# Performance work log

Measured on AMD Instinct MI355X. Metric: run time of the kernel, lower is better.

The kernel has to match this reference:

```python
import jax, jax.numpy as jnp
import numpy as np
import math

N_HEADS = 16
D_EMB = 1024
D_HEAD = D_EMB // N_HEADS


def setup_inputs() -> dict:
    key = jax.random.key(0)
    ks = jax.random.split(key, 5)
    scale_in = 1.0 / math.sqrt(D_EMB)
    x = jax.random.normal(ks[0], (2, 2048, D_EMB), dtype=jnp.float32)
    w_in = jax.random.uniform(ks[1], (3 * D_EMB, D_EMB), dtype=jnp.float32, minval=-scale_in, maxval=scale_in)
    b_in = jax.random.uniform(ks[2], (3 * D_EMB,), dtype=jnp.float32, minval=-scale_in, maxval=scale_in)
    w_out = jax.random.uniform(ks[3], (D_EMB, D_EMB), dtype=jnp.float32, minval=-scale_in, maxval=scale_in)
    b_out = jax.random.uniform(ks[4], (D_EMB,), dtype=jnp.float32, minval=-scale_in, maxval=scale_in)
    return {"x": x, "w_in": w_in, "b_in": b_in, "w_out": w_out, "b_out": b_out, "apply_mask": 1}


def reference(x, w_in, b_in, w_out, b_out, apply_mask):
    B, S, D = x.shape
    # fused QKV projection: torch Linear uses y = x @ W^T + b
    qkv = jnp.einsum('bsd,ed->bse', x, w_in) + b_in  # [B,S,3D]
    q, k, v = jnp.split(qkv, 3, axis=-1)
    # [B,H,S,Dh]
    q = q.reshape(B, S, N_HEADS, D_HEAD).transpose(0, 2, 1, 3)
    k = k.reshape(B, S, N_HEADS, D_HEAD).transpose(0, 2, 1, 3)
    v = v.reshape(B, S, N_HEADS, D_HEAD).transpose(0, 2, 1, 3)
    w = jnp.einsum('bhqd,bhkd->bhqk', q, k)  # [B,H,S,S]
    if apply_mask:
        causal = jnp.triu(jnp.ones((S, S), dtype=bool), k=1)
        w = jnp.where(causal, -jnp.inf, w)
    w = w / jnp.sqrt(jnp.float32(D_HEAD)).astype(w.dtype)
    w = jax.nn.softmax(w, axis=-1)
    score = jnp.einsum('bhqk,bhkd->bhqd', w, v)  # [B,H,S,Dh]
    score = score.transpose(0, 2, 1, 3).reshape(B, S, D)
    return jnp.einsum('bsd,ed->bse', score, w_out) + b_out
```

## Files before the change

kernel.cpp:

```cpp
#include <hip/hip_runtime.h>
#include <stdint.h>

#define DEMB 1024
#define NHEAD 16
#define DHEAD 64
#define SEQ 2048
#define MROWS 4096

typedef __bf16 bf16x8 __attribute__((ext_vector_type(8)));
typedef float f32x4 __attribute__((ext_vector_type(4)));
typedef unsigned short u16;

#define LOG2E 1.44269504088896340736f

__device__ __forceinline__ u16 f2b(float f) {
  uint32_t u = __builtin_bit_cast(uint32_t, f);
  u += 0x7fffu + ((u >> 16) & 1u);
  return (u16)(u >> 16);
}

__device__ __forceinline__ f32x4 mfma16(bf16x8 a, bf16x8 b, f32x4 c) {
  return __builtin_amdgcn_mfma_f32_16x16x32_bf16(a, b, c, 0, 0, 0);
}

__device__ __forceinline__ void gload_lds16(const void* g, void* l) {
  __builtin_amdgcn_global_load_lds(
      (__attribute__((address_space(1))) unsigned int*)(g),
      (__attribute__((address_space(3))) unsigned int*)(l), 16, 0, 0);
}

__device__ __forceinline__ void tile_barrier() {
  __builtin_amdgcn_sched_barrier(0);
  asm volatile("s_waitcnt vmcnt(0) lgkmcnt(0)" ::: "memory");
  __builtin_amdgcn_s_barrier();
  __builtin_amdgcn_sched_barrier(0);
}

__global__ void cvt3_f32_bf16(const float* __restrict__ a, int na,
                              const float* __restrict__ b, int nb,
                              const float* __restrict__ c, int nc,
                              u16* __restrict__ da, u16* __restrict__ db,
                              u16* __restrict__ dc) {
  const int total = (na + nb + nc) >> 2;
  const int stride = gridDim.x * blockDim.x;
  for (int t = blockIdx.x * blockDim.x + threadIdx.x; t < total; t += stride) {
    int i = t << 2;
    const float* s;
    u16* d;
    if (i < na) {
      s = a + i; d = da + i;
    } else if (i < na + nb) {
      s = b + (i - na); d = db + (i - na);
    } else {
      s = c + (i - na - nb); d = dc + (i - na - nb);
    }
    float4 f = *(const float4*)s;
    ushort4 o;
    o.x = f2b(f.x); o.y = f2b(f.y); o.z = f2b(f.z); o.w = f2b(f.w);
    *(ushort4*)d = o;
  }
}

template <int EPI>
__global__ __launch_bounds__(256, 2) void gemm_nt(
    const u16* __restrict__ A, const u16* __restrict__ Bw,
    const float* __restrict__ bias, int K, int N,
    u16* __restrict__ q_out, u16* __restrict__ k_out, u16* __restrict__ v_out,
    float* __restrict__ f_out) {
  __shared__ __align__(16) u16 As[128 * 64];
  __shared__ __align__(16) u16 Bs[128 * 64];
  const int tid = threadIdx.x;
  const int w = tid >> 6;
  const int lane = tid & 63;
  const int wm = w >> 1, wn = w & 1;
  const int m0 = blockIdx.y * 128, n0 = blockIdx.x * 128;
  const int l16 = lane & 15, lg = lane >> 4;
  const int st_row = lane >> 3, st_slot = lane & 7;

  f32x4 acc[4][4] = {};

  for (int k0 = 0; k0 < K; k0 += 64) {
#pragma unroll
    for (int i = 0; i < 4; ++i) {
      const int chunk = (w << 2) | i;
      const int row = (chunk << 3) | st_row;
      const int scol = (st_slot ^ (row & 7)) << 3;
      gload_lds16(A + (size_t)(m0 + row) * K + k0 + scol, (char*)As + (chunk << 10));
      gload_lds16(Bw + (size_t)(n0 + row) * K + k0 + scol, (char*)Bs + (chunk << 10));
    }
    __syncthreads();
#pragma unroll
    for (int ks = 0; ks < 2; ++ks) {
      bf16x8 af[4], bfr[4];
#pragma unroll
      for (int mi = 0; mi < 4; ++mi) {
        const int row = wm * 64 + mi * 16 + l16;
        const int cb = ((ks << 6) | (lg << 4)) ^ ((row & 7) << 4);
        af[mi] = *(const bf16x8*)((const char*)As + row * 128 + cb);
      }
#pragma unroll
      for (int ni = 0; ni < 4; ++ni) {
        const int row = wn * 64 + ni * 16 + l16;
        const int cb = ((ks << 6) | (lg << 4)) ^ ((row & 7) << 4);
        bfr[ni] = *(const bf16x8*)((const char*)Bs + row * 128 + cb);
      }
#pragma unroll
      for (int mi = 0; mi < 4; ++mi)
#pragma unroll
        for (int ni = 0; ni < 4; ++ni)
          acc[mi][ni] = mfma16(af[mi], bfr[ni], acc[mi][ni]);
    }
    __syncthreads();
  }

#pragma unroll
  for (int ni = 0; ni < 4; ++ni) {
    const int n = n0 + wn * 64 + ni * 16 + l16;
    const float bv = bias[n];
    if (EPI == 0) {
      const int part = n >> 10;
      const int hh = (n >> 6) & 15;
      const int dh = n & 63;
      const float scl = (part == 0) ? (0.125f * LOG2E) : 1.0f;
      u16* dst = (part == 0) ? q_out : (part == 1) ? k_out : v_out;
#pragma unroll
      for (int mi = 0; mi < 4; ++mi) {
#pragma unroll
        for (int i = 0; i < 4; ++i) {
          const int m = m0 + wm * 64 + mi * 16 + (lg << 2) + i;
          const int bq = m >> 11, s = m & 2047;
          dst[((size_t)((bq << 4) | hh) * SEQ + s) * DHEAD + dh] = f2b((acc[mi][ni][i] + bv) * scl);
        }
      }
    } else {
#pragma unroll
      for (int mi = 0; mi < 4; ++mi)
#pragma unroll
        for (int i = 0; i < 4; ++i) {
          const int m = m0 + wm * 64 + mi * 16 + (lg << 2) + i;
          f_out[(size_t)m * N + n] = acc[mi][ni][i] + bv;
        }
    }
  }
}

__device__ __forceinline__ void stage_k(const u16* __restrict__ Kb, size_t base,
                                        int jt, u16* Ks, int w, int lane) {
  const int st_row = lane >> 3, st_slot = lane & 7;
#pragma unroll
  for (int i = 0; i < 2; ++i) {
    const int chunk = (w << 1) | i;
    const int row = (chunk << 3) | st_row;
    const int scol = (st_slot ^ (row & 7)) << 3;
    gload_lds16(Kb + base + (size_t)(jt * 64 + row) * DHEAD + scol, (char*)Ks + (chunk << 10));
  }
}

__device__ __forceinline__ int vswz(int rt) {
  return ((rt & 7) ^ ((rt >> 3) & 7)) << 4;
}

__device__ __forceinline__ void write_vt(u16* Vt, uint4 va, uint4 vb, int tid) {
  const int c0 = (tid & 7) << 3;
  const int vr0 = tid >> 3;
  const int vr1 = 32 + (tid >> 3);
  const u16* pa = (const u16*)&va;
  const u16* pb = (const u16*)&vb;
#pragma unroll
  for (int e = 0; e < 8; ++e) {
    const int rt = c0 + e;
    const int sw = vswz(rt);
    *(u16*)((char*)Vt + rt * 128 + ((vr0 << 1) ^ sw)) = pa[e];
    *(u16*)((char*)Vt + rt * 128 + ((vr1 << 1) ^ sw)) = pb[e];
  }
}

__global__ __launch_bounds__(256, 4) void attn_fwd(
    const u16* __restrict__ Qb, const u16* __restrict__ Kb,
    const u16* __restrict__ Vb, u16* __restrict__ Ob,
    const int* __restrict__ amask) {
  __shared__ __align__(16) u16 Ks[2][64 * 64];
  __shared__ __align__(16) u16 Vt[2][64 * 64];
  __shared__ __align__(16) uint32_t Ps[4][16 * 32];
  const int tid = threadIdx.x;
  const int w = tid >> 6, lane = tid & 63;
  const int l16 = lane & 15, lg = lane >> 4;

  const int id = blockIdx.x;
  const int xcd = id & 7;
  const int r = id >> 3;
  const int bh = (xcd << 2) | (r & 3);
  const int p = r >> 2;
  const int qiA = 31 - p, qiB = p;

  const size_t base = (size_t)bh * (SEQ * DHEAD);
  const bool causal = (amask[0] != 0);
  const int ntA = causal ? (qiA + 1) : (SEQ / 64);
  const int ntB = causal ? (qiB + 1) : (SEQ / 64);
  const int nt = ntA + ntB;
  const int b = bh >> 4, h = bh & 15;

  int qseg0 = qiA * 64;

  bf16x8 qf[2];
  {
    const u16* qp = Qb + base + (size_t)(qseg0 + (w << 4) + l16) * DHEAD + (lg << 3);
    qf[0] = *(const bf16x8*)qp;
    qf[1] = *(const bf16x8*)(qp + 32);
  }

  float mrow = -1e30f, lrow = 0.f;
  f32x4 oacc[4] = {};

  const int vcol = (tid & 7) << 3;
  const int vrow = tid >> 3;
  const int key = (l16 & 7) << 2;
  char* prow = (char*)(&Ps[w][0]) + l16 * 128;

  stage_k(Kb, base, 0, Ks[0], w, lane);
  {
    uint4 va = *(const uint4*)(Vb + base + (size_t)vrow * DHEAD + vcol);
    uint4 vb2 = *(const uint4*)(Vb + base + (size_t)(32 + vrow) * DHEAD + vcol);
    write_vt(Vt[0], va, vb2, tid);
  }
  tile_barrier();

  int cur = 0;
  for (int t = 0; t < nt; ++t) {
    const int j = (t >= ntA) ? (t - ntA) : t;
    const u16* Kcur = Ks[cur];
    const u16* Vcur = Vt[cur];
    const bool pre = (t + 1 < nt);
    uint4 vna = {}, vnb = {};
    if (pre) {
      const int jn = (t + 1 >= ntA) ? (t + 1 - ntA) : (t + 1);
      stage_k(Kb, base, jn, Ks[cur ^ 1], w, lane);
      const u16* vsrc = Vb + base + (size_t)jn * 64 * DHEAD;
      vna = *(const uint4*)(vsrc + (size_t)vrow * DHEAD + vcol);
      vnb = *(const uint4*)(vsrc + (size_t)(32 + vrow) * DHEAD + vcol);
    }

    f32x4 sv[4];
    __builtin_amdgcn_s_setprio(1);
#pragma unroll
    for (int nf = 0; nf < 4; ++nf) {
      const int row = nf * 16 + l16;
      const int sw = (row & 7) << 4;
      bf16x8 kf0 = *(const bf16x8*)((const char*)Kcur + row * 128 + ((lg << 4) ^ sw));
      bf16x8 kf1 = *(const bf16x8*)((const char*)Kcur + row * 128 + ((64 | (lg << 4)) ^ sw));
      f32x4 s = {};
      s = mfma16(kf0, qf[0], s);
      s = mfma16(kf1, qf[1], s);
      sv[nf] = s;
    }
    __builtin_amdgcn_s_setprio(0);

    const bool segEnd = (t == ntA - 1) || (t == nt - 1);
    if (causal && segEnd) {
      const int q = qseg0 + (w << 4) + l16;
#pragma unroll
      for (int nf = 0; nf < 4; ++nf)
#pragma unroll
        for (int i = 0; i < 4; ++i) {
          const int kv = j * 64 + nf * 16 + (lg << 2) + i;
          if (kv > q) sv[nf][i] = -1e30f;
        }
    }

    float tmax;
    {
      float t0 = fmaxf(fmaxf(sv[0][0], sv[0][1]), fmaxf(sv[0][2], sv[0][3]));
      float t1 = fmaxf(fmaxf(sv[1][0], sv[1][1]), fmaxf(sv[1][2], sv[1][3]));
      float t2 = fmaxf(fmaxf(sv[2][0], sv[2][1]), fmaxf(sv[2][2], sv[2][3]));
      float t3 = fmaxf(fmaxf(sv[3][0], sv[3][1]), fmaxf(sv[3][2], sv[3][3]));
      tmax = fmaxf(fmaxf(t0, t1), fmaxf(t2, t3));
      tmax = fmaxf(tmax, __shfl_xor(tmax, 16));
      tmax = fmaxf(tmax, __shfl_xor(tmax, 32));
    }

    if (__any(tmax > mrow + 8.0f)) {
      const float mnew = fmaxf(mrow, tmax);
      const float corr = exp2f(mrow - mnew);
      mrow = mnew;
      lrow *= corr;
#pragma unroll
      for (int df = 0; df < 4; ++df)
#pragma unroll
        for (int i = 0; i < 4; ++i) oacc[df][i] *= corr;
    }

    float psum = 0.f;
#pragma unroll
    for (int nf = 0; nf < 4; ++nf) {
      const float p0 = exp2f(sv[nf][0] - mrow);
      const float p1 = exp2f(sv[nf][1] - mrow);
      const float p2 = exp2f(sv[nf][2] - mrow);
      const float p3 = exp2f(sv[nf][3] - mrow);
      psum += (p0 + p1) + (p2 + p3);
      uint2 pk;
      pk.x = f2b(p0) | ((uint32_t)f2b(p1) << 16);
      pk.y = f2b(p2) | ((uint32_t)f2b(p3) << 16);
      const int word = ((nf << 3) | (lg << 1)) ^ key;
      *(uint2*)(prow + word * 4) = pk;
    }
    psum += __shfl_xor(psum, 16);
    psum += __shfl_xor(psum, 32);
    lrow += psum;

    bf16x8 pa0 = *(const bf16x8*)(prow + ((((lg << 2)) ^ key) << 2));
    bf16x8 pa1 = *(const bf16x8*)(prow + (((16 | (lg << 2)) ^ key) << 2));

    __builtin_amdgcn_s_setprio(1);
#pragma unroll
    for (int df = 0; df < 4; ++df) {
      const int row = df * 16 + l16;
      const int sw = vswz(row);
      bf16x8 vf0 = *(const bf16x8*)((const char*)Vcur + row * 128 + ((lg << 4) ^ sw));
      bf16x8 vf1 = *(const bf16x8*)((const char*)Vcur + row * 128 + ((64 | (lg << 4)) ^ sw));
      oacc[df] = mfma16(vf0, pa0, oacc[df]);
      oacc[df] = mfma16(vf1, pa1, oacc[df]);
    }
    __builtin_amdgcn_s_setprio(0);

    if (segEnd) {
      const float inv = 1.0f / lrow;
      const int s = qseg0 + (w << 4) + l16;
      u16* orow = Ob + (size_t)(b * SEQ + s) * DEMB + h * DHEAD;
#pragma unroll
      for (int df = 0; df < 4; ++df) {
        ushort4 o;
        o.x = f2b(oacc[df][0] * inv);
        o.y = f2b(oacc[df][1] * inv);
        o.z = f2b(oacc[df][2] * inv);
        o.w = f2b(oacc[df][3] * inv);
        *(ushort4*)(orow + df * 16 + (lg << 2)) = o;
      }
      if (t != nt - 1) {
        qseg0 = qiB * 64;
        mrow = -1e30f;
        lrow = 0.f;
#pragma unroll
        for (int df = 0; df < 4; ++df)
#pragma unroll
          for (int i = 0; i < 4; ++i) oacc[df][i] = 0.f;
        const u16* qp = Qb + base + (size_t)(qseg0 + (w << 4) + l16) * DHEAD + (lg << 3);
        qf[0] = *(const bf16x8*)qp;
        qf[1] = *(const bf16x8*)(qp + 32);
      }
    }

    if (pre) {
      write_vt(Vt[cur ^ 1], vna, vnb, tid);
      tile_barrier();
    }
    cur ^= 1;
  }
}

extern "C" void kernel_launch(void* const* d_in, const int* in_sizes, int n_in,
                              void* d_out, int out_size, void* d_ws, size_t ws_size,
                              hipStream_t stream) {
  const float* x = (const float*)d_in[0];
  const float* w_in = (const float*)d_in[1];
  const float* b_in = (const float*)d_in[2];
  const float* w_out = (const float*)d_in[3];
  const float* b_out = (const float*)d_in[4];
  const int* amask = (const int*)d_in[5];
  float* out = (float*)d_out;

  u16* xb = (u16*)d_ws;
  u16* wib = xb + (size_t)MROWS * DEMB;
  u16* wob = wib + (size_t)3 * DEMB * DEMB;
  u16* Qb = wob + (size_t)DEMB * DEMB;
  u16* Kb = Qb + (size_t)MROWS * DEMB;
  u16* Vb = Kb + (size_t)MROWS * DEMB;
  u16* Ab = xb;

  cvt3_f32_bf16<<<2048, 256, 0, stream>>>(x, MROWS * DEMB, w_in, 3 * DEMB * DEMB,
                                          w_out, DEMB * DEMB, xb, wib, wob);

  gemm_nt<0><<<dim3(24, 32), 256, 0, stream>>>(xb, wib, b_in, DEMB, 3 * DEMB,
                                               Qb, Kb, Vb, nullptr);
  attn_fwd<<<512, 256, 0, stream>>>(Qb, Kb, Vb, Ab, amask);
  gemm_nt<1><<<dim3(8, 32), 256, 0, stream>>>(Ab, wob, b_out, DEMB, DEMB,
                                              nullptr, nullptr, nullptr, out);
}
```

Before: 118.6 us.

## Widen attention KV tile to 128 keys with new swizzled LDS layout

Doubles the key/value tile per iteration from 64 to 128, halving the loop trip count and the number of barriers per Q block. K staging and the transposed V layout get a new 16-slot XOR swizzle, and the P buffer is doubled. Launch bounds drop from 4 to 2 blocks per CU to fit the larger LDS use. It also switches to the hardware exp2 intrinsic and the native bf16 conversion. The causal diagonal tile now masks a 128-wide block, adding some wasted work on the diagonal, and occupancy is lower.

```diff
diff --git a/kernel.cpp b/kernel.cpp
--- a/kernel.cpp
+++ b/kernel.cpp
@@ -14,9 +14,10 @@
 #define LOG2E 1.44269504088896340736f
 
 __device__ __forceinline__ u16 f2b(float f) {
-  uint32_t u = __builtin_bit_cast(uint32_t, f);
-  u += 0x7fffu + ((u >> 16) & 1u);
-  return (u16)(u >> 16);
+  return __builtin_bit_cast(u16, (__bf16)f);
+}
+__device__ __forceinline__ uint32_t pk2(float a, float b) {
+  return (uint32_t)f2b(a) | ((uint32_t)f2b(b) << 16);
 }
 
 __device__ __forceinline__ f32x4 mfma16(bf16x8 a, bf16x8 b, f32x4 c) {
@@ -144,44 +145,44 @@
   }
 }
 
+__device__ __forceinline__ int swz4(int r) { return (r ^ (r >> 3)) & 15; }
+
 __device__ __forceinline__ void stage_k(const u16* __restrict__ Kb, size_t base,
                                         int jt, u16* Ks, int w, int lane) {
-  const int st_row = lane >> 3, st_slot = lane & 7;
-#pragma unroll
-  for (int i = 0; i < 2; ++i) {
-    const int chunk = (w << 1) | i;
-    const int row = (chunk << 3) | st_row;
-    const int scol = (st_slot ^ (row & 7)) << 3;
-    gload_lds16(Kb + base + (size_t)(jt * 64 + row) * DHEAD + scol, (char*)Ks + (chunk << 10));
-  }
-}
-
-__device__ __forceinline__ int vswz(int rt) {
-  return ((rt & 7) ^ ((rt >> 3) & 7)) << 4;
-}
-
-__device__ __forceinline__ void write_vt(u16* Vt, uint4 va, uint4 vb, int tid) {
+#pragma unroll
+  for (int i = 0; i < 4; ++i) {
+    const int g = (w << 2) | i;
+    const int row = (g << 2) | (lane >> 4);
+    const int shat = (lane & 15) ^ swz4(row);
+    const int kv = (row << 1) | (shat >> 3);
+    const int del = (shat & 7) << 3;
+    gload_lds16(Kb + base + (size_t)(jt * 128 + kv) * DHEAD + del,
+                (char*)Ks + (g << 10));
+  }
+}
+
+__device__ __forceinline__ void write_vt(u16* Vt, const uint4* v, int tid) {
   const int c0 = (tid & 7) << 3;
-  const int vr0 = tid >> 3;
-  const int vr1 = 32 + (tid >> 3);
-  const u16* pa = (const u16*)&va;
-  const u16* pb = (const u16*)&vb;
-#pragma unroll
-  for (int e = 0; e < 8; ++e) {
-    const int rt = c0 + e;
-    const int sw = vswz(rt);
-    *(u16*)((char*)Vt + rt * 128 + ((vr0 << 1) ^ sw)) = pa[e];
-    *(u16*)((char*)Vt + rt * 128 + ((vr1 << 1) ^ sw)) = pb[e];
-  }
-}
-
-__global__ __launch_bounds__(256, 4) void attn_fwd(
+  const int vrb = tid >> 3;
+#pragma unroll
+  for (int k = 0; k < 4; ++k) {
+    const int vr = vrb + (k << 5);
+    const u16* pv = (const u16*)&v[k];
+#pragma unroll
+    for (int e = 0; e < 8; ++e) {
+      const int rt = c0 + e;
+      *(u16*)((char*)Vt + rt * 256 + ((vr << 1) ^ (swz4(rt) << 4))) = pv[e];
+    }
+  }
+}
+
+__global__ __launch_bounds__(256, 2) void attn_fwd(
     const u16* __restrict__ Qb, const u16* __restrict__ Kb,
     const u16* __restrict__ Vb, u16* __restrict__ Ob,
     const int* __restrict__ amask) {
-  __shared__ __align__(16) u16 Ks[2][64 * 64];
-  __shared__ __align__(16) u16 Vt[2][64 * 64];
-  __shared__ __align__(16) uint32_t Ps[4][16 * 32];
+  __shared__ __align__(16) u16 Ks[2][64 * 128];
+  __shared__ __align__(16) u16 Vt[2][64 * 128];
+  __shared__ __align__(16) uint32_t Ps[4][1024];
   const int tid = threadIdx.x;
   const int w = tid >> 6, lane = tid & 63;
   const int l16 = lane & 15, lg = lane >> 4;
@@ -195,8 +196,8 @@
 
   const size_t base = (size_t)bh * (SEQ * DHEAD);
   const bool causal = (amask[0] != 0);
-  const int ntA = causal ? (qiA + 1) : (SEQ / 64);
-  const int ntB = causal ? (qiB + 1) : (SEQ / 64);
+  const int ntA = causal ? ((qiA >> 1) + 1) : (SEQ / 128);
+  const int ntB = causal ? ((qiB >> 1) + 1) : (SEQ / 128);
   const int nt = ntA + ntB;
   const int b = bh >> 4, h = bh & 15;
 
@@ -215,13 +216,15 @@
   const int vcol = (tid & 7) << 3;
   const int vrow = tid >> 3;
   const int key = (l16 & 7) << 2;
-  char* prow = (char*)(&Ps[w][0]) + l16 * 128;
+  char* prow = (char*)(&Ps[w][0]) + l16 * 256;
 
   stage_k(Kb, base, 0, Ks[0], w, lane);
   {
-    uint4 va = *(const uint4*)(Vb + base + (size_t)vrow * DHEAD + vcol);
-    uint4 vb2 = *(const uint4*)(Vb + base + (size_t)(32 + vrow) * DHEAD + vcol);
-    write_vt(Vt[0], va, vb2, tid);
+    uint4 v[4];
+#pragma unroll
+    for (int k = 0; k < 4; ++k)
+      v[k] = *(const uint4*)(Vb + base + (size_t)(vrow + (k << 5)) * DHEAD + vcol);
+    write_vt(Vt[0], v, tid);
   }
   tile_barrier();
 
@@ -231,23 +234,25 @@
     const u16* Kcur = Ks[cur];
     const u16* Vcur = Vt[cur];
     const bool pre = (t + 1 < nt);
-    uint4 vna = {}, vnb = {};
+    uint4 vn[4] = {};
     if (pre) {
       const int jn = (t + 1 >= ntA) ? (t + 1 - ntA) : (t + 1);
       stage_k(Kb, base, jn, Ks[cur ^ 1], w, lane);
-      const u16* vsrc = Vb + base + (size_t)jn * 64 * DHEAD;
-      vna = *(const uint4*)(vsrc + (size_t)vrow * DHEAD + vcol);
-      vnb = *(const uint4*)(vsrc + (size_t)(32 + vrow) * DHEAD + vcol);
-    }
-
-    f32x4 sv[4];
+      const u16* vsrc = Vb + base + (size_t)jn * 128 * DHEAD;
+#pragma unroll
+      for (int k = 0; k < 4; ++k)
+        vn[k] = *(const uint4*)(vsrc + (size_t)(vrow + (k << 5)) * DHEAD + vcol);
+    }
+
+    f32x4 sv[8];
     __builtin_amdgcn_s_setprio(1);
 #pragma unroll
-    for (int nf = 0; nf < 4; ++nf) {
-      const int row = nf * 16 + l16;
-      const int sw = (row & 7) << 4;
-      bf16x8 kf0 = *(const bf16x8*)((const char*)Kcur + row * 128 + ((lg << 4) ^ sw));
-      bf16x8 kf1 = *(const bf16x8*)((const char*)Kcur + row * 128 + ((64 | (lg << 4)) ^ sw));
+    for (int nf = 0; nf < 8; ++nf) {
+      const int row2 = (nf << 3) | (l16 >> 1);
+      const int sz = swz4(row2);
+      const int s0 = ((l16 & 1) << 3) | lg;
+      bf16x8 kf0 = *(const bf16x8*)((const char*)Kcur + row2 * 256 + ((s0 ^ sz) << 4));
+      bf16x8 kf1 = *(const bf16x8*)((const char*)Kcur + row2 * 256 + (((s0 | 4) ^ sz) << 4));
       f32x4 s = {};
       s = mfma16(kf0, qf[0], s);
       s = mfma16(kf1, qf[1], s);
@@ -259,28 +264,35 @@
     if (causal && segEnd) {
       const int q = qseg0 + (w << 4) + l16;
 #pragma unroll
-      for (int nf = 0; nf < 4; ++nf)
+      for (int nf = 0; nf < 8; ++nf)
 #pragma unroll
         for (int i = 0; i < 4; ++i) {
-          const int kv = j * 64 + nf * 16 + (lg << 2) + i;
+          const int kv = j * 128 + (nf << 4) + (lg << 2) + i;
           if (kv > q) sv[nf][i] = -1e30f;
         }
     }
 
     float tmax;
     {
-      float t0 = fmaxf(fmaxf(sv[0][0], sv[0][1]), fmaxf(sv[0][2], sv[0][3]));
-      float t1 = fmaxf(fmaxf(sv[1][0], sv[1][1]), fmaxf(sv[1][2], sv[1][3]));
-      float t2 = fmaxf(fmaxf(sv[2][0], sv[2][1]), fmaxf(sv[2][2], sv[2][3]));
-      float t3 = fmaxf(fmaxf(sv[3][0], sv[3][1]), fmaxf(sv[3][2], sv[3][3]));
-      tmax = fmaxf(fmaxf(t0, t1), fmaxf(t2, t3));
+      f32x4 m01, m23, m45, m67, ma, mb, mt;
+#pragma unroll
+      for (int i = 0; i < 4; ++i) {
+        m01[i] = fmaxf(sv[0][i], sv[1][i]);
+        m23[i] = fmaxf(sv[2][i], sv[3][i]);
+        m45[i] = fmaxf(sv[4][i], sv[5][i]);
+        m67[i] = fmaxf(sv[6][i], sv[7][i]);
+        ma[i] = fmaxf(m01[i], m23[i]);
+        mb[i] = fmaxf(m45[i], m67[i]);
+        mt[i] = fmaxf(ma[i], mb[i]);
+      }
+      tmax = fmaxf(fmaxf(mt[0], mt[1]), fmaxf(mt[2], mt[3]));
       tmax = fmaxf(tmax, __shfl_xor(tmax, 16));
       tmax = fmaxf(tmax, __shfl_xor(tmax, 32));
     }
 
     if (__any(tmax > mrow + 8.0f)) {
       const float mnew = fmaxf(mrow, tmax);
-      const float corr = exp2f(mrow - mnew);
+      const float corr = __builtin_amdgcn_exp2f(mrow - mnew);
       mrow = mnew;
       lrow *= corr;
 #pragma unroll
@@ -289,36 +301,41 @@
         for (int i = 0; i < 4; ++i) oacc[df][i] *= corr;
     }
 
-    float psum = 0.f;
-#pragma unroll
-    for (int nf = 0; nf < 4; ++nf) {
-      const float p0 = exp2f(sv[nf][0] - mrow);
-      const float p1 = exp2f(sv[nf][1] - mrow);
-      const float p2 = exp2f(sv[nf][2] - mrow);
-      const float p3 = exp2f(sv[nf][3] - mrow);
-      psum += (p0 + p1) + (p2 + p3);
-      uint2 pk;
-      pk.x = f2b(p0) | ((uint32_t)f2b(p1) << 16);
-      pk.y = f2b(p2) | ((uint32_t)f2b(p3) << 16);
+    float ps0 = 0.f, ps1 = 0.f;
+#pragma unroll
+    for (int nf = 0; nf < 8; ++nf) {
+      const float p0 = __builtin_amdgcn_exp2f(sv[nf][0] - mrow);
+      const float p1 = __builtin_amdgcn_exp2f(sv[nf][1] - mrow);
+      const float p2 = __builtin_amdgcn_exp2f(sv[nf][2] - mrow);
+      const float p3 = __builtin_amdgcn_exp2f(sv[nf][3] - mrow);
+      ps0 += p0 + p1;
+      ps1 += p2 + p3;
+      uint2 pkv;
+      pkv.x = pk2(p0, p1);
+      pkv.y = pk2(p2, p3);
       const int word = ((nf << 3) | (lg << 1)) ^ key;
-      *(uint2*)(prow + word * 4) = pk;
-    }
+      *(uint2*)(prow + word * 4) = pkv;
+    }
+    float psum = ps0 + ps1;
     psum += __shfl_xor(psum, 16);
     psum += __shfl_xor(psum, 32);
     lrow += psum;
 
-    bf16x8 pa0 = *(const bf16x8*)(prow + ((((lg << 2)) ^ key) << 2));
-    bf16x8 pa1 = *(const bf16x8*)(prow + (((16 | (lg << 2)) ^ key) << 2));
+    bf16x8 pa[4];
+#pragma unroll
+    for (int s = 0; s < 4; ++s)
+      pa[s] = *(const bf16x8*)(prow + ((((s << 4) | (lg << 2)) ^ key) << 2));
 
     __builtin_amdgcn_s_setprio(1);
 #pragma unroll
     for (int df = 0; df < 4; ++df) {
-      const int row = df * 16 + l16;
-      const int sw = vswz(row);
-      bf16x8 vf0 = *(const bf16x8*)((const char*)Vcur + row * 128 + ((lg << 4) ^ sw));
-      bf16x8 vf1 = *(const bf16x8*)((const char*)Vcur + row * 128 + ((64 | (lg << 4)) ^ sw));
-      oacc[df] = mfma16(vf0, pa0, oacc[df]);
-      oacc[df] = mfma16(vf1, pa1, oacc[df]);
+      const int row = (df << 4) + l16;
+      const int sz = swz4(row) << 4;
+#pragma unroll
+      for (int s = 0; s < 4; ++s) {
+        bf16x8 vf = *(const bf16x8*)((const char*)Vcur + row * 256 + (((s << 6) | (lg << 4)) ^ sz));
+        oacc[df] = mfma16(vf, pa[s], oacc[df]);
+      }
     }
     __builtin_amdgcn_s_setprio(0);
 
@@ -333,7 +350,7 @@
         o.y = f2b(oacc[df][1] * inv);
         o.z = f2b(oacc[df][2] * inv);
         o.w = f2b(oacc[df][3] * inv);
-        *(ushort4*)(orow + df * 16 + (lg << 2)) = o;
+        *(ushort4*)(orow + (df << 4) + (lg << 2)) = o;
       }
       if (t != nt - 1) {
         qseg0 = qiB * 64;
@@ -350,7 +367,7 @@
     }
 
     if (pre) {
-      write_vt(Vt[cur ^ 1], vna, vnb, tid);
+      write_vt(Vt[cur ^ 1], vn, tid);
       tile_barrier();
     }
     cur ^= 1;
```

Measured after the change: 111.8 us. 5.7% less time.
